# Performance work log

Measured on AMD Instinct MI355X. Metric: run time of the kernel, lower is better.

The kernel has to match this reference:

```python
import jax, jax.numpy as jnp
import numpy as np

D = 128      # internal_dimensions
L = 4        # num_edge_convs
N = 100000   # nodes
E = 800000   # edges
G = 64       # graphs
IN = 4       # in_channels


def _ln(x, g, b):
    m = jnp.mean(x, -1, keepdims=True)
    v = jnp.mean((x - m) ** 2, -1, keepdims=True)
    return (x - m) * jax.lax.rsqrt(v + 1e-5) * g + b


def _gelu(x):
    return jax.nn.gelu(x, approximate=False)  # torch nn.GELU default (erf)


def _seg_mean(x, seg, n):
    s = jax.ops.segment_sum(x, seg, num_segments=n)
    c = jax.ops.segment_sum(jnp.ones((x.shape[0], 1), x.dtype), seg, num_segments=n)
    return s / jnp.maximum(c, 1.0)


def _seg_max(x, seg, n):
    m = jax.ops.segment_max(x, seg, num_segments=n)
    return jnp.where(jnp.isfinite(m), m, 0.0)  # empty segments -> 0 (PyG convention)


def _forward(x, edge_index, batch, num_graphs,
             in_W1, in_b1, in_g1, in_bn1, in_W2, in_b2, in_g2, in_bn2,
             pre_g, pre_b, cW1, cb1, cg1, cbb1, cW2, cb2, cg2, cbb2, pW, pb,
             ag_g, ag_b,
             kW1, kb1, kg1, kbb1, kW2, kb2, kg2, kbb2,
             kW3, kb3, kg3, kbb3, kW4, kb4):
    n = x.shape[0]
    # input_net: Linear -> LN -> GELU -> Linear -> LN   (dropout=0, eval)
    h = _gelu(_ln(x @ in_W1 + in_b1, in_g1, in_bn1))
    h = _ln(h @ in_W2 + in_b2, in_g2, in_bn2)

    x_in_max = _seg_max(h, batch, num_graphs)
    x_in_mean = _seg_mean(h, batch, num_graphs)

    src, dst = edge_index[0], edge_index[1]  # PyG: message from src (x_j) to dst (x_i)
    xcur = h
    for l in range(L):
        identity = xcur
        hn = _ln(xcur, pre_g[l], pre_b[l])
        xi = hn[dst]            # [E, D]
        xj = hn[src]            # [E, D]
        m = jnp.concatenate([xi, xj - xi], axis=-1)       # [E, 2D]
        m = _gelu(_ln(m @ cW1[l] + cb1[l], cg1[l], cbb1[l]))
        m = _gelu(_ln(m @ cW2[l] + cb2[l], cg2[l], cbb2[l]))
        a_max = _seg_max(m, dst, n)
        a_mean = _seg_mean(m, dst, n)
        aggr = jnp.concatenate([a_max, a_mean], axis=-1)  # [N, 2D]
        xcur = identity + aggr @ pW[l] + pb[l]

    xcur = _ln(xcur, ag_g, ag_b)
    x_g_max = _seg_max(xcur, batch, num_graphs)
    x_g_mean = _seg_mean(xcur, batch, num_graphs)

    xp = jnp.concatenate([x_in_max, x_in_mean, x_g_max, x_g_mean], axis=-1)  # [G, 4D]
    z = _gelu(_ln(xp @ kW1 + kb1, kg1, kbb1))
    z = _gelu(_ln(z @ kW2 + kb2, kg2, kbb2))
    z = _gelu(_ln(z @ kW3 + kb3, kg3, kbb3))
    return z @ kW4 + kb4  # [G, 1]


def setup_inputs() -> dict:
    key = jax.random.key(0)
    ks = iter(jax.random.split(key, 64))
    def W(shape, fan):
        return jax.random.normal(next(ks), shape, jnp.float32) * np.float32((2.0 / fan) ** 0.5)
    inp = {}
    inp["x"] = jax.random.normal(next(ks), (N, IN), jnp.float32)
    inp["edge_index"] = jax.random.randint(next(ks), (2, E), 0, N)
    inp["batch"] = jnp.sort(jax.random.randint(next(ks), (N,), 0, G))
    inp["num_graphs"] = G
    inp["in_W1"] = W((IN, D), IN); inp["in_b1"] = jnp.zeros((D,), jnp.float32)
    inp["in_g1"] = jnp.ones((D,), jnp.float32); inp["in_bn1"] = jnp.zeros((D,), jnp.float32)
    inp["in_W2"] = W((D, D), D); inp["in_b2"] = jnp.zeros((D,), jnp.float32)
    inp["in_g2"] = jnp.ones((D,), jnp.float32); inp["in_bn2"] = jnp.zeros((D,), jnp.float32)
    inp["pre_g"] = jnp.ones((L, D), jnp.float32); inp["pre_b"] = jnp.zeros((L, D), jnp.float32)
    inp["cW1"] = W((L, 2 * D, D), 2 * D); inp["cb1"] = jnp.zeros((L, D), jnp.float32)
    inp["cg1"] = jnp.ones((L, D), jnp.float32); inp["cbb1"] = jnp.zeros((L, D), jnp.float32)
    inp["cW2"] = W((L, D, D), D); inp["cb2"] = jnp.zeros((L, D), jnp.float32)
    inp["cg2"] = jnp.ones((L, D), jnp.float32); inp["cbb2"] = jnp.zeros((L, D), jnp.float32)
    inp["pW"] = W((L, 2 * D, D), 2 * D); inp["pb"] = jnp.zeros((L, D), jnp.float32)
    inp["ag_g"] = jnp.ones((D,), jnp.float32); inp["ag_b"] = jnp.zeros((D,), jnp.float32)
    inp["kW1"] = W((4 * D, D), 4 * D); inp["kb1"] = jnp.zeros((D,), jnp.float32)
    inp["kg1"] = jnp.ones((D,), jnp.float32); inp["kbb1"] = jnp.zeros((D,), jnp.float32)
    inp["kW2"] = W((D, D), D); inp["kb2"] = jnp.zeros((D,), jnp.float32)
    inp["kg2"] = jnp.ones((D,), jnp.float32); inp["kbb2"] = jnp.zeros((D,), jnp.float32)
    inp["kW3"] = W((D, D // 4), D); inp["kb3"] = jnp.zeros((D // 4,), jnp.float32)
    inp["kg3"] = jnp.ones((D // 4,), jnp.float32); inp["kbb3"] = jnp.zeros((D // 4,), jnp.float32)
    inp["kW4"] = W((D // 4, 1), D // 4); inp["kb4"] = jnp.zeros((1,), jnp.float32)
    return inp


def reference(x, edge_index, batch, num_graphs,
              in_W1, in_b1, in_g1, in_bn1, in_W2, in_b2, in_g2, in_bn2,
              pre_g, pre_b, cW1, cb1, cg1, cbb1, cW2, cb2, cg2, cbb2, pW, pb,
              ag_g, ag_b,
              kW1, kb1, kg1, kbb1, kW2, kb2, kg2, kbb2,
              kW3, kb3, kg3, kbb3, kW4, kb4):
    return _forward(x, edge_index, batch, num_graphs,
                    in_W1, in_b1, in_g1, in_bn1, in_W2, in_b2, in_g2, in_bn2,
                    pre_g, pre_b, cW1, cb1, cg1, cbb1, cW2, cb2, cg2, cbb2, pW, pb,
                    ag_g, ag_b,
                    kW1, kb1, kg1, kbb1, kW2, kb2, kg2, kbb2,
                    kW3, kb3, kg3, kbb3, kW4, kb4)
```

## Files before the change

### kernel.cpp

```cpp
#include <hip/hip_runtime.h>
#include <hip/hip_bf16.h>
#include <math.h>

#define MAPNEGINF 0x007FFFFFu

__device__ __forceinline__ float geluf(float x) {
    return 0.5f * x * (1.0f + erff(x * 0.70710678118654752f));
}
__device__ __forceinline__ unsigned fmap(float f) {
    unsigned u = __float_as_uint(f);
    return ((int)u < 0) ? ~u : (u | 0x80000000u);
}
__device__ __forceinline__ float funmap(unsigned m) {
    return __uint_as_float((m & 0x80000000u) ? (m ^ 0x80000000u) : ~m);
}
__device__ __forceinline__ float wred64(float v) {
#pragma unroll
    for (int m = 1; m < 64; m <<= 1) v += __shfl_xor(v, m);
    return v;
}

__device__ __forceinline__ void stage_wq(float* Ws, const float* __restrict__ src, int t) {
#pragma unroll
    for (int it = 0; it < 4; ++it) {
        const int idx = it * 1024 + (t << 2);
        *(float4*)(Ws + idx) = *(const float4*)(src + idx);
    }
}

__device__ __forceinline__ void kloop_q(const float* As, const float* Ws, float (&acc)[4][8],
                                        const int r0, const int ogc, const int kb) {
#pragma unroll
    for (int kk = 0; kk < 32; kk += 4) {
        const float4 a0 = *(const float4*)(As + (r0 + 0) * 132 + kb + kk);
        const float4 a1 = *(const float4*)(As + (r0 + 1) * 132 + kb + kk);
        const float4 a2 = *(const float4*)(As + (r0 + 2) * 132 + kb + kk);
        const float4 a3 = *(const float4*)(As + (r0 + 3) * 132 + kb + kk);
#define MAD8(R, AV)                                                                     \
    {                                                                                   \
        acc[R][0] += (AV)*wA.x; acc[R][1] += (AV)*wA.y; acc[R][2] += (AV)*wA.z;         \
        acc[R][3] += (AV)*wA.w; acc[R][4] += (AV)*wB.x; acc[R][5] += (AV)*wB.y;         \
        acc[R][6] += (AV)*wB.z; acc[R][7] += (AV)*wB.w;                                 \
    }
#define KSTEP(J, C)                                                                     \
    {                                                                                   \
        const float4 wA = *(const float4*)(Ws + (kk + (J)) * 128 + ogc);                \
        const float4 wB = *(const float4*)(Ws + (kk + (J)) * 128 + 64 + ogc);           \
        MAD8(0, a0.C) MAD8(1, a1.C) MAD8(2, a2.C) MAD8(3, a3.C)                         \
    }
        KSTEP(0, x) KSTEP(1, y) KSTEP(2, z) KSTEP(3, w)
#undef KSTEP
#undef MAD8
    }
}

__global__ void k_zero(unsigned* __restrict__ p, int n) {
    const int i = blockIdx.x * 256 + threadIdx.x;
    if (i < n) p[i] = 0u;
}

__global__ void k_count(const int* __restrict__ ei, unsigned* __restrict__ deg, int E) {
    const int e = blockIdx.x * 256 + threadIdx.x;
    if (e < E) atomicAdd(deg + ei[E + e], 1u);
}

__global__ void k_scan1(const unsigned* __restrict__ deg, unsigned* __restrict__ excl,
                        unsigned* __restrict__ bsum, int n) {
    __shared__ unsigned sh[256];
    const int t = threadIdx.x;
    const int base = blockIdx.x * 1024 + t * 4;
    unsigned v0 = (base + 0 < n) ? deg[base + 0] : 0u;
    unsigned v1 = (base + 1 < n) ? deg[base + 1] : 0u;
    unsigned v2 = (base + 2 < n) ? deg[base + 2] : 0u;
    unsigned v3 = (base + 3 < n) ? deg[base + 3] : 0u;
    const unsigned s = v0 + v1 + v2 + v3;
    sh[t] = s;
    __syncthreads();
    for (int off = 1; off < 256; off <<= 1) {
        unsigned x = 0;
        if (t >= off) x = sh[t - off];
        __syncthreads();
        if (t >= off) sh[t] += x;
        __syncthreads();
    }
    const unsigned ebase = sh[t] - s;
    if (base + 0 < n) excl[base + 0] = ebase;
    if (base + 1 < n) excl[base + 1] = ebase + v0;
    if (base + 2 < n) excl[base + 2] = ebase + v0 + v1;
    if (base + 3 < n) excl[base + 3] = ebase + v0 + v1 + v2;
    if (t == 255) bsum[blockIdx.x] = sh[255];
}

__global__ void k_scan2(unsigned* __restrict__ bsum, int nb) {
    __shared__ unsigned sh[256];
    const int t = threadIdx.x;
    const unsigned v = (t < nb) ? bsum[t] : 0u;
    sh[t] = v;
    __syncthreads();
    for (int off = 1; off < 256; off <<= 1) {
        unsigned x = 0;
        if (t >= off) x = sh[t - off];
        __syncthreads();
        if (t >= off) sh[t] += x;
        __syncthreads();
    }
    if (t < nb) bsum[t] = sh[t] - v;
}

__global__ void k_scan3(unsigned* __restrict__ excl, const unsigned* __restrict__ bsum, int n) {
    const int t = threadIdx.x;
    const int base = blockIdx.x * 1024 + t * 4;
    const unsigned add = bsum[blockIdx.x];
#pragma unroll
    for (int j = 0; j < 4; ++j)
        if (base + j < n) excl[base + j] += add;
}

__global__ void k_scatter(const int* __restrict__ ei, unsigned* __restrict__ cursor,
                          int* __restrict__ eperm, int E) {
    const int e = blockIdx.x * 256 + threadIdx.x;
    if (e < E) {
        const unsigned pos = atomicAdd(cursor + ei[E + e], 1u);
        eperm[pos] = e;
    }
}

__global__ void k_in1(const float* __restrict__ x, const float* __restrict__ W1,
                      const float* __restrict__ b1, const float* __restrict__ g1,
                      const float* __restrict__ bn1, float* __restrict__ h, int n) {
    const int t = threadIdx.x, lane = t & 63, wave = t >> 6;
    const int d0 = lane << 1;
    const float2 w0 = *(const float2*)(W1 + d0);
    const float2 w1 = *(const float2*)(W1 + 128 + d0);
    const float2 w2 = *(const float2*)(W1 + 256 + d0);
    const float2 w3 = *(const float2*)(W1 + 384 + d0);
    const float2 bb = *(const float2*)(b1 + d0);
    const float2 gg = *(const float2*)(g1 + d0);
    const float2 nn = *(const float2*)(bn1 + d0);
    const int stride = gridDim.x * 4;
    for (int node = blockIdx.x * 4 + wave; node < n; node += stride) {
        const float4 xv = *(const float4*)(x + (size_t)node * 4);
        float h0 = bb.x + xv.x * w0.x + xv.y * w1.x + xv.z * w2.x + xv.w * w3.x;
        float h1 = bb.y + xv.x * w0.y + xv.y * w1.y + xv.z * w2.y + xv.w * w3.y;
        const float s = wred64(h0 + h1), q = wred64(h0 * h0 + h1 * h1);
        const float mean = s * 0.0078125f, var = q * 0.0078125f - mean * mean;
        const float rs = rsqrtf(var + 1e-5f);
        h0 = geluf((h0 - mean) * rs * gg.x + nn.x);
        h1 = geluf((h1 - mean) * rs * gg.y + nn.y);
        *(float2*)(h + (size_t)node * 128 + d0) = make_float2(h0, h1);
    }
}

__global__ __launch_bounds__(256, 2) void k_in2(const float* __restrict__ A,
                                                const float* __restrict__ W,
                                                const float* __restrict__ bias,
                                                const float* __restrict__ g,
                                                const float* __restrict__ b,
                                                float* __restrict__ C, int n) {
    __shared__ float As[64 * 132];
    __shared__ float Ws[4096];
    const int t = threadIdx.x;
    const int n0 = blockIdx.x * 64;
    {
        const int r = t >> 2, c0 = (t & 3) << 5;
        const int row = n0 + r;
        const bool ok = row < n;
#pragma unroll
        for (int j = 0; j < 8; ++j) {
            const int col = c0 + (j << 2);
            float4 v = make_float4(0.f, 0.f, 0.f, 0.f);
            if (ok) v = *(const float4*)(A + (size_t)row * 128 + col);
            *(float4*)(As + r * 132 + col) = v;
        }
    }
    float acc[4][8];
#pragma unroll
    for (int r = 0; r < 4; ++r)
#pragma unroll
        for (int o = 0; o < 8; ++o) acc[r][o] = 0.f;
    const int og = t & 15, eg = t >> 4;
    const int ogc = og << 2, r0 = eg << 2;
#pragma unroll
    for (int q4 = 0; q4 < 4; ++q4) {
        stage_wq(Ws, W + q4 * 4096, t);
        __syncthreads();
        kloop_q(As, Ws, acc, r0, ogc, q4 * 32);
        __syncthreads();
    }
    const float4 bA = *(const float4*)(bias + ogc);
    const float4 bB = *(const float4*)(bias + 64 + ogc);
    const float4 gA = *(const float4*)(g + ogc);
    const float4 gB = *(const float4*)(g + 64 + ogc);
    const float4 lA = *(const float4*)(b + ogc);
    const float4 lB = *(const float4*)(b + 64 + ogc);
#pragma unroll
    for (int r = 0; r < 4; ++r) {
        float v[8];
        v[0] = acc[r][0] + bA.x; v[1] = acc[r][1] + bA.y;
        v[2] = acc[r][2] + bA.z; v[3] = acc[r][3] + bA.w;
        v[4] = acc[r][4] + bB.x; v[5] = acc[r][5] + bB.y;
        v[6] = acc[r][6] + bB.z; v[7] = acc[r][7] + bB.w;
        float s = 0.f, q = 0.f;
#pragma unroll
        for (int o = 0; o < 8; ++o) { s += v[o]; q += v[o] * v[o]; }
#pragma unroll
        for (int m = 1; m < 16; m <<= 1) { s += __shfl_xor(s, m); q += __shfl_xor(q, m); }
        const float mean = s * 0.0078125f;
        const float var = q * 0.0078125f - mean * mean;
        const float rs = rsqrtf(var + 1e-5f);
        const int row = n0 + r0 + r;
        if (row < n) {
            *(float4*)(C + (size_t)row * 128 + ogc) = make_float4(
                (v[0] - mean) * rs * gA.x + lA.x, (v[1] - mean) * rs * gA.y + lA.y,
                (v[2] - mean) * rs * gA.z + lA.z, (v[3] - mean) * rs * gA.w + lA.w);
            *(float4*)(C + (size_t)row * 128 + 64 + ogc) = make_float4(
                (v[4] - mean) * rs * gB.x + lB.x, (v[5] - mean) * rs * gB.y + lB.y,
                (v[6] - mean) * rs * gB.z + lB.z, (v[7] - mean) * rs * gB.w + lB.w);
        }
    }
}

__global__ void k_ln(const float* __restrict__ in, const float* __restrict__ g,
                     const float* __restrict__ b, float* __restrict__ out, int n) {
    const int t = threadIdx.x, lane = t & 63, wave = t >> 6;
    const int d0 = lane << 1;
    const float ga = g[d0], gb = g[d0 + 1], ba = b[d0], bb = b[d0 + 1];
    const int stride = gridDim.x * 4;
    for (int node = blockIdx.x * 4 + wave; node < n; node += stride) {
        const float2 v = *(const float2*)(in + (size_t)node * 128 + d0);
        const float s = wred64(v.x + v.y), q = wred64(v.x * v.x + v.y * v.y);
        const float mean = s * 0.0078125f, var = q * 0.0078125f - mean * mean;
        const float rs = rsqrtf(var + 1e-5f);
        *(float2*)(out + (size_t)node * 128 + d0) =
            make_float2((v.x - mean) * rs * ga + ba, (v.y - mean) * rs * gb + bb);
    }
}

__global__ void k_wxj(const float* __restrict__ c, float* __restrict__ Wx,
                      float* __restrict__ Wj) {
    const int idx = blockIdx.x * 256 + threadIdx.x;
    const float a = c[idx], b = c[16384 + idx];
    Wx[idx] = a - b;
    Wj[idx] = b;
}

__global__ void k_fill(unsigned* __restrict__ amax, float* __restrict__ asum, int n4) {
    const uint4 mneg = make_uint4(MAPNEGINF, MAPNEGINF, MAPNEGINF, MAPNEGINF);
    const float4 z = make_float4(0.f, 0.f, 0.f, 0.f);
    for (int i = blockIdx.x * blockDim.x + threadIdx.x; i < n4; i += gridDim.x * blockDim.x) {
        ((uint4*)amax)[i] = mneg;
        ((float4*)asum)[i] = z;
    }
}

__global__ __launch_bounds__(256, 2) void k_pq(const float* __restrict__ xcur,
                                               const float* __restrict__ g,
                                               const float* __restrict__ b,
                                               const float* __restrict__ Wx,
                                               const float* __restrict__ Wj,
                                               const float* __restrict__ cb1,
                                               float* __restrict__ P, float* __restrict__ Q,
                                               int n) {
    __shared__ float As[64 * 132];
    __shared__ float Ws[4096];
    __shared__ float sg[128], sb[128];
    const int t = threadIdx.x;
    const int n0 = blockIdx.x * 64;
    if (t < 128) { sg[t] = g[t]; sb[t] = b[t]; }
    __syncthreads();
    {
        const int r = t >> 2, c0 = (t & 3) << 5;
        const int row = n0 + r;
        const bool ok = row < n;
        float4 v4[8];
        float s = 0.f, q = 0.f;
        if (ok) {
#pragma unroll
            for (int j = 0; j < 8; ++j) {
                v4[j] = *(const float4*)(xcur + (size_t)row * 128 + c0 + (j << 2));
                s += v4[j].x + v4[j].y + v4[j].z + v4[j].w;
                q += v4[j].x * v4[j].x + v4[j].y * v4[j].y + v4[j].z * v4[j].z +
                     v4[j].w * v4[j].w;
            }
        } else {
#pragma unroll
            for (int j = 0; j < 8; ++j) v4[j] = make_float4(0.f, 0.f, 0.f, 0.f);
        }
        s += __shfl_xor(s, 1); s += __shfl_xor(s, 2);
        q += __shfl_xor(q, 1); q += __shfl_xor(q, 2);
        const float mean = s * 0.0078125f;
        const float var = q * 0.0078125f - mean * mean;
        const float rs = rsqrtf(var + 1e-5f);
#pragma unroll
        for (int j = 0; j < 8; ++j) {
            const int c = c0 + (j << 2);
            As[r * 132 + c + 0] = (v4[j].x - mean) * rs * sg[c + 0] + sb[c + 0];
            As[r * 132 + c + 1] = (v4[j].y - mean) * rs * sg[c + 1] + sb[c + 1];
            As[r * 132 + c + 2] = (v4[j].z - mean) * rs * sg[c + 2] + sb[c + 2];
            As[r * 132 + c + 3] = (v4[j].w - mean) * rs * sg[c + 3] + sb[c + 3];
        }
    }
    float accP[4][8], accQ[4][8];
#pragma unroll
    for (int r = 0; r < 4; ++r)
#pragma unroll
        for (int o = 0; o < 8; ++o) { accP[r][o] = 0.f; accQ[r][o] = 0.f; }
    const int og = t & 15, eg = t >> 4;
    const int ogc = og << 2, r0 = eg << 2;
#pragma unroll
    for (int q4 = 0; q4 < 4; ++q4) {
        stage_wq(Ws, Wx + q4 * 4096, t);
        __syncthreads();
        kloop_q(As, Ws, accP, r0, ogc, q4 * 32);
        __syncthreads();
    }
#pragma unroll
    for (int q4 = 0; q4 < 4; ++q4) {
        stage_wq(Ws, Wj + q4 * 4096, t);
        __syncthreads();
        kloop_q(As, Ws, accQ, r0, ogc, q4 * 32);
        __syncthreads();
    }
    const float4 bA = *(const float4*)(cb1 + ogc);
    const float4 bB = *(const float4*)(cb1 + 64 + ogc);
#pragma unroll
    for (int r = 0; r < 4; ++r) {
        const int row = n0 + r0 + r;
        if (row < n) {
            *(float4*)(P + (size_t)row * 128 + ogc) =
                make_float4(accP[r][0] + bA.x, accP[r][1] + bA.y, accP[r][2] + bA.z,
                            accP[r][3] + bA.w);
            *(float4*)(P + (size_t)row * 128 + 64 + ogc) =
                make_float4(accP[r][4] + bB.x, accP[r][5] + bB.y, accP[r][6] + bB.z,
                            accP[r][7] + bB.w);
            *(float4*)(Q + (size_t)row * 128 + ogc) =
                make_float4(accQ[r][0], accQ[r][1], accQ[r][2], accQ[r][3]);
            *(float4*)(Q + (size_t)row * 128 + 64 + ogc) =
                make_float4(accQ[r][4], accQ[r][5], accQ[r][6], accQ[r][7]);
        }
    }
}

__global__ __launch_bounds__(256, 2) void k_edge(
    const float* __restrict__ P, const float* __restrict__ Q, const int* __restrict__ ei,
    const int* __restrict__ eperm, const float* __restrict__ W2, const float* __restrict__ g1,
    const float* __restrict__ b1, const float* __restrict__ cb2, const float* __restrict__ g2,
    const float* __restrict__ b2, unsigned* __restrict__ amax, float* __restrict__ asum, int E) {
    __shared__ float Us[64 * 132];
    __shared__ float Ws[4096];
    __shared__ int sdst[64], ssrc[64], sdg[64];
    __shared__ float scb2[128], sg2[128], sb2[128];
    const int t = threadIdx.x;
    const int base = blockIdx.x * 64;
    if (base >= E) return;
    if (t < 64) {
        const int idx = base + t;
        const int e = eperm[idx < E ? idx : (E - 1)];
        ssrc[t] = ei[e];
        const int d = ei[E + e];
        sdg[t] = d;
        sdst[t] = (idx < E) ? d : -1;
    }
    if (t >= 128) {
        const int d = t - 128;
        scb2[d] = cb2[d];
        sg2[d] = g2[d];
        sb2[d] = b2[d];
    }
    __syncthreads();
    const int lane = t & 63, wave = t >> 6;
    const int d0 = lane << 1;
    const float g1a = g1[d0], g1b = g1[d0 + 1], b1a = b1[d0], b1b = b1[d0 + 1];
#pragma unroll 2
    for (int p = 0; p < 16; ++p) {
        const int i = (p << 2) + wave;
        const int nd = sdg[i], ns = ssrc[i];
        const float2 pv = *(const float2*)(P + (size_t)nd * 128 + d0);
        const float2 qv = *(const float2*)(Q + (size_t)ns * 128 + d0);
        const float x0 = pv.x + qv.x, x1 = pv.y + qv.y;
        const float s = wred64(x0 + x1);
        const float q = wred64(x0 * x0 + x1 * x1);
        const float mean = s * 0.0078125f;
        const float var = q * 0.0078125f - mean * mean;
        const float rs = rsqrtf(var + 1e-5f);
        const float y0 = geluf((x0 - mean) * rs * g1a + b1a);
        const float y1 = geluf((x1 - mean) * rs * g1b + b1b);
        *(float2*)(Us + i * 132 + d0) = make_float2(y0, y1);
    }
    float acc[4][8];
#pragma unroll
    for (int r = 0; r < 4; ++r)
#pragma unroll
        for (int o = 0; o < 8; ++o) acc[r][o] = 0.f;
    const int og = t & 15, eg = t >> 4;
    const int ogc = og << 2, r0 = eg << 2;
#pragma unroll
    for (int q4 = 0; q4 < 4; ++q4) {
        stage_wq(Ws, W2 + q4 * 4096, t);
        __syncthreads();
        kloop_q(Us, Ws, acc, r0, ogc, q4 * 32);
        __syncthreads();
    }
#pragma unroll
    for (int r = 0; r < 4; ++r) {
        float v[8];
        float s = 0.f, q = 0.f;
#pragma unroll
        for (int o = 0; o < 8; ++o) {
            const int col = (o < 4) ? (ogc + o) : (64 + ogc + o - 4);
            v[o] = acc[r][o] + scb2[col];
            s += v[o];
            q += v[o] * v[o];
        }
#pragma unroll
        for (int m = 1; m < 16; m <<= 1) { s += __shfl_xor(s, m); q += __shfl_xor(q, m); }
        const float mean = s * 0.0078125f;
        const float var = q * 0.0078125f - mean * mean;
        const float rs = rsqrtf(var + 1e-5f);
#pragma unroll
        for (int o = 0; o < 8; ++o) {
            const int col = (o < 4) ? (ogc + o) : (64 + ogc + o - 4);
            v[o] = geluf((v[o] - mean) * rs * sg2[col] + sb2[col]);
        }
        *(float4*)(Us + (r0 + r) * 132 + ogc) = make_float4(v[0], v[1], v[2], v[3]);
        *(float4*)(Us + (r0 + r) * 132 + 64 + ogc) = make_float4(v[4], v[5], v[6], v[7]);
    }
    __syncthreads();
    if (t < 128) {
        int cur = sdst[0];
        float vmax = -INFINITY, vsum = 0.f;
        for (int i = 0; i < 64; ++i) {
            const int dn = sdst[i];
            if (dn != cur) {
                if (cur >= 0) {
                    atomicMax(amax + (size_t)cur * 128 + t, fmap(vmax));
                    atomicAdd(asum + (size_t)cur * 128 + t, vsum);
                }
                cur = dn;
                vmax = -INFINITY;
                vsum = 0.f;
            }
            const float v = Us[i * 132 + t];
            vmax = fmaxf(vmax, v);
            vsum += v;
        }
        if (cur >= 0) {
            atomicMax(amax + (size_t)cur * 128 + t, fmap(vmax));
            atomicAdd(asum + (size_t)cur * 128 + t, vsum);
        }
    }
}

__global__ __launch_bounds__(256, 2) void k_update(const unsigned* __restrict__ amax,
                                                   const float* __restrict__ asum,
                                                   const unsigned* __restrict__ deg,
                                                   const float* __restrict__ pW,
                                                   const float* __restrict__ pb,
                                                   float* __restrict__ xcur, int n) {
    __shared__ float As[64 * 132];
    __shared__ float Ws[4096];
    const int t = threadIdx.x;
    const int n0 = blockIdx.x * 64;
    const int og = t & 15, eg = t >> 4;
    const int ogc = og << 2, r0 = eg << 2;
    float acc[4][8];
#pragma unroll
    for (int r = 0; r < 4; ++r)
#pragma unroll
        for (int o = 0; o < 8; ++o) acc[r][o] = 0.f;
    const int r = t >> 2, c0 = (t & 3) << 5;
    const int row = n0 + r;
    const bool ok = row < n;
#pragma unroll
    for (int pass = 0; pass < 2; ++pass) {
        if (pass == 0) {
#pragma unroll
            for (int j = 0; j < 8; ++j) {
                const int col = c0 + (j << 2);
                float4 v = make_float4(0.f, 0.f, 0.f, 0.f);
                if (ok) {
                    const uint4 u = *(const uint4*)(amax + (size_t)row * 128 + col);
                    v.x = (u.x == MAPNEGINF) ? 0.f : funmap(u.x);
                    v.y = (u.y == MAPNEGINF) ? 0.f : funmap(u.y);
                    v.z = (u.z == MAPNEGINF) ? 0.f : funmap(u.z);
                    v.w = (u.w == MAPNEGINF) ? 0.f : funmap(u.w);
                }
                *(float4*)(As + r * 132 + col) = v;
            }
        } else {
            float inv = 0.f;
            if (ok) {
                const unsigned dv = deg[row];
                inv = 1.f / (float)(dv < 1u ? 1u : dv);
            }
#pragma unroll
            for (int j = 0; j < 8; ++j) {
                const int col = c0 + (j << 2);
                float4 v = make_float4(0.f, 0.f, 0.f, 0.f);
                if (ok) {
                    const float4 sv = *(const float4*)(asum + (size_t)row * 128 + col);
                    v = make_float4(sv.x * inv, sv.y * inv, sv.z * inv, sv.w * inv);
                }
                *(float4*)(As + r * 132 + col) = v;
            }
        }
#pragma unroll
        for (int q4 = 0; q4 < 4; ++q4) {
            stage_wq(Ws, pW + (size_t)(pass * 128 + q4 * 32) * 128, t);
            __syncthreads();
            kloop_q(As, Ws, acc, r0, ogc, q4 * 32);
            __syncthreads();
        }
    }
    const float4 bA = *(const float4*)(pb + ogc);
    const float4 bB = *(const float4*)(pb + 64 + ogc);
#pragma unroll
    for (int rr = 0; rr < 4; ++rr) {
        const int orow = n0 + r0 + rr;
        if (orow < n) {
            const float4 x0 = *(const float4*)(xcur + (size_t)orow * 128 + ogc);
            const float4 x1 = *(const float4*)(xcur + (size_t)orow * 128 + 64 + ogc);
            *(float4*)(xcur + (size_t)orow * 128 + ogc) =
                make_float4(x0.x + acc[rr][0] + bA.x, x0.y + acc[rr][1] + bA.y,
                            x0.z + acc[rr][2] + bA.z, x0.w + acc[rr][3] + bA.w);
            *(float4*)(xcur + (size_t)orow * 128 + 64 + ogc) =
                make_float4(x1.x + acc[rr][4] + bB.x, x1.y + acc[rr][5] + bB.y,
                            x1.z + acc[rr][6] + bB.z, x1.w + acc[rr][7] + bB.w);
        }
    }
}

__global__ void k_pool_init(unsigned* __restrict__ gmax1, float* __restrict__ gsum1,
                            unsigned* __restrict__ gcount1, unsigned* __restrict__ gmax2,
                            float* __restrict__ gsum2, unsigned* __restrict__ gcount2, int ng) {
    const int i = blockIdx.x * 256 + threadIdx.x;
    if (i < ng * 128) {
        gmax1[i] = MAPNEGINF;
        gsum1[i] = 0.f;
        gmax2[i] = MAPNEGINF;
        gsum2[i] = 0.f;
    }
    if (i < ng) {
        gcount1[i] = 0u;
        gcount2[i] = 0u;
    }
}

__global__ void k_pool(const float* __restrict__ in, const int* __restrict__ batch,
                       unsigned* __restrict__ gmax, float* __restrict__ gsum,
                       unsigned* __restrict__ gcount, int n) {
    const int t = threadIdx.x;
    if (t >= 128) return;
    const int per = (n + gridDim.x - 1) / gridDim.x;
    const int i0 = blockIdx.x * per;
    const int i1 = min(n, i0 + per);
    if (i0 >= i1) return;
    int cur = batch[i0];
    float vmax = -INFINITY, vsum = 0.f;
    unsigned cnt = 0;
    for (int i = i0; i < i1; ++i) {
        const int g = batch[i];
        if (g != cur) {
            atomicMax(gmax + (size_t)cur * 128 + t, fmap(vmax));
            atomicAdd(gsum + (size_t)cur * 128 + t, vsum);
            if (t == 0) atomicAdd(gcount + cur, cnt);
            cur = g;
            vmax = -INFINITY;
            vsum = 0.f;
            cnt = 0;
        }
        const float v = in[(size_t)i * 128 + t];
        vmax = fmaxf(vmax, v);
        vsum += v;
        cnt++;
    }
    atomicMax(gmax + (size_t)cur * 128 + t, fmap(vmax));
    atomicAdd(gsum + (size_t)cur * 128 + t, vsum);
    if (t == 0) atomicAdd(gcount + cur, cnt);
}

__global__ void k_xp(const unsigned* __restrict__ gmax1, const float* __restrict__ gsum1,
                     const unsigned* __restrict__ gcount1, const unsigned* __restrict__ gmax2,
                     const float* __restrict__ gsum2, const unsigned* __restrict__ gcount2,
                     float* __restrict__ xp) {
    const int g = blockIdx.x, d = threadIdx.x;
    const unsigned c1u = gcount1[g], c2u = gcount2[g];
    const float c1 = (float)(c1u < 1u ? 1u : c1u);
    const float c2 = (float)(c2u < 1u ? 1u : c2u);
    const unsigned m1 = gmax1[g * 128 + d], m2 = gmax2[g * 128 + d];
    xp[g * 512 + d] = (m1 == MAPNEGINF) ? 0.f : funmap(m1);
    xp[g * 512 + 128 + d] = gsum1[g * 128 + d] / c1;
    xp[g * 512 + 256 + d] = (m2 == MAPNEGINF) ? 0.f : funmap(m2);
    xp[g * 512 + 384 + d] = gsum2[g * 128 + d] / c2;
}

__global__ __launch_bounds__(64) void k_know(
    const float* __restrict__ xp, const float* __restrict__ kW1, const float* __restrict__ kb1,
    const float* __restrict__ kg1, const float* __restrict__ kbb1, const float* __restrict__ kW2,
    const float* __restrict__ kb2, const float* __restrict__ kg2, const float* __restrict__ kbb2,
    const float* __restrict__ kW3, const float* __restrict__ kb3, const float* __restrict__ kg3,
    const float* __restrict__ kbb3, const float* __restrict__ kW4, const float* __restrict__ kb4,
    float* __restrict__ out) {
    __shared__ float sh[512];
    __shared__ float s3[32];
    const int l = threadIdx.x, g = blockIdx.x;
    const int d0 = l << 1;
    *(float4*)(sh + l * 8) = *(const float4*)(xp + g * 512 + l * 8);
    *(float4*)(sh + l * 8 + 4) = *(const float4*)(xp + g * 512 + l * 8 + 4);
    __syncthreads();
    float a0 = kb1[d0], a1 = kb1[d0 + 1];
    for (int k = 0; k < 512; ++k) {
        const float u = sh[k];
        const float2 w = *(const float2*)(kW1 + k * 128 + d0);
        a0 += u * w.x;
        a1 += u * w.y;
    }
    {
        const float s = wred64(a0 + a1), q = wred64(a0 * a0 + a1 * a1);
        const float mean = s * 0.0078125f, var = q * 0.0078125f - mean * mean;
        const float rs = rsqrtf(var + 1e-5f);
        a0 = geluf((a0 - mean) * rs * kg1[d0] + kbb1[d0]);
        a1 = geluf((a1 - mean) * rs * kg1[d0 + 1] + kbb1[d0 + 1]);
    }
    __syncthreads();
    sh[d0] = a0;
    sh[d0 + 1] = a1;
    __syncthreads();
    float b0v = kb2[d0], b1v = kb2[d0 + 1];
    for (int k = 0; k < 128; ++k) {
        const float u = sh[k];
        const float2 w = *(const float2*)(kW2 + k * 128 + d0);
        b0v += u * w.x;
        b1v += u * w.y;
    }
    {
        const float s = wred64(b0v + b1v), q = wred64(b0v * b0v + b1v * b1v);
        const float mean = s * 0.0078125f, var = q * 0.0078125f - mean * mean;
        const float rs = rsqrtf(var + 1e-5f);
        b0v = geluf((b0v - mean) * rs * kg2[d0] + kbb2[d0]);
        b1v = geluf((b1v - mean) * rs * kg2[d0 + 1] + kbb2[d0 + 1]);
    }
    __syncthreads();
    sh[d0] = b0v;
    sh[d0 + 1] = b1v;
    __syncthreads();
    const int d3 = (l & 15) << 1;
    float c0 = kb3[d3], c1 = kb3[d3 + 1];
    for (int k = 0; k < 128; ++k) {
        const float u = sh[k];
        const float2 w = *(const float2*)(kW3 + k * 32 + d3);
        c0 += u * w.x;
        c1 += u * w.y;
    }
    {
        float s = c0 + c1, q = c0 * c0 + c1 * c1;
#pragma unroll
        for (int m = 1; m < 16; m <<= 1) {
            s += __shfl_xor(s, m);
            q += __shfl_xor(q, m);
        }
        const float mean = s * 0.03125f, var = q * 0.03125f - mean * mean;
        const float rs = rsqrtf(var + 1e-5f);
        c0 = geluf((c0 - mean) * rs * kg3[d3] + kbb3[d3]);
        c1 = geluf((c1 - mean) * rs * kg3[d3 + 1] + kbb3[d3 + 1]);
    }
    if (l < 16) {
        s3[d3] = c0;
        s3[d3 + 1] = c1;
    }
    __syncthreads();
    if (l == 0) {
        float rr = kb4[0];
        for (int k = 0; k < 32; ++k) rr += s3[k] * kW4[k];
        out[g] = rr;
    }
}

extern "C" void kernel_launch(void* const* d_in, const int* in_sizes, int n_in, void* d_out,
                              int out_size, void* d_ws, size_t ws_size, hipStream_t stream) {
    const int N = in_sizes[0] / 4;
    const int E = in_sizes[1] / 2;
    const int G = 64;
    const int L = 4;

    const float* x = (const float*)d_in[0];
    const int* ei = (const int*)d_in[1];
    const int* batch = (const int*)d_in[2];
    const float* inW1 = (const float*)d_in[4];
    const float* inb1 = (const float*)d_in[5];
    const float* ing1 = (const float*)d_in[6];
    const float* inbn1 = (const float*)d_in[7];
    const float* inW2 = (const float*)d_in[8];
    const float* inb2 = (const float*)d_in[9];
    const float* ing2 = (const float*)d_in[10];
    const float* inbn2 = (const float*)d_in[11];
    const float* pre_g = (const float*)d_in[12];
    const float* pre_b = (const float*)d_in[13];
    const float* cW1 = (const float*)d_in[14];
    const float* cb1 = (const float*)d_in[15];
    const float* cg1 = (const float*)d_in[16];
    const float* cbb1 = (const float*)d_in[17];
    const float* cW2 = (const float*)d_in[18];
    const float* cb2 = (const float*)d_in[19];
    const float* cg2 = (const float*)d_in[20];
    const float* cbb2 = (const float*)d_in[21];
    const float* pW = (const float*)d_in[22];
    const float* pb = (const float*)d_in[23];
    const float* ag_g = (const float*)d_in[24];
    const float* ag_b = (const float*)d_in[25];
    const float* kW1 = (const float*)d_in[26];
    const float* kb1 = (const float*)d_in[27];
    const float* kg1 = (const float*)d_in[28];
    const float* kbb1 = (const float*)d_in[29];
    const float* kW2 = (const float*)d_in[30];
    const float* kb2 = (const float*)d_in[31];
    const float* kg2 = (const float*)d_in[32];
    const float* kbb2 = (const float*)d_in[33];
    const float* kW3 = (const float*)d_in[34];
    const float* kb3 = (const float*)d_in[35];
    const float* kg3 = (const float*)d_in[36];
    const float* kbb3 = (const float*)d_in[37];
    const float* kW4 = (const float*)d_in[38];
    const float* kb4 = (const float*)d_in[39];
    float* out = (float*)d_out;

    char* wsb = (char*)d_ws;
    size_t off = 0;
    auto ALC = [&](size_t bytes) {
        void* p = wsb + off;
        off = (off + bytes + 255) & ~(size_t)255;
        return p;
    };
    const size_t NB = (size_t)N * 128 * 4;
    float* xcur = (float*)ALC(NB);
    float* Pb = (float*)ALC(NB);
    float* Qb = (float*)ALC(NB);
    unsigned* amax = (unsigned*)ALC(NB);
    float* asum = (float*)ALC(NB);
    unsigned* deg = (unsigned*)ALC((size_t)N * 4);
    unsigned* cursor = (unsigned*)ALC((size_t)N * 4);
    unsigned* bsum = (unsigned*)ALC(4096);
    int* eperm = (int*)ALC((size_t)E * 4);
    float* Wx = (float*)ALC(65536);
    float* Wj = (float*)ALC(65536);
    unsigned* gmax1 = (unsigned*)ALC((size_t)G * 128 * 4);
    float* gsum1 = (float*)ALC((size_t)G * 128 * 4);
    unsigned* gcount1 = (unsigned*)ALC((size_t)G * 4);
    unsigned* gmax2 = (unsigned*)ALC((size_t)G * 128 * 4);
    float* gsum2 = (float*)ALC((size_t)G * 128 * 4);
    unsigned* gcount2 = (unsigned*)ALC((size_t)G * 4);
    float* xp = (float*)ALC((size_t)G * 512 * 4);

    if (off > ws_size) {
        k_zero<<<(out_size + 255) / 256, 256, 0, stream>>>((unsigned*)d_out, out_size);
        return;
    }

    k_zero<<<(N + 255) / 256, 256, 0, stream>>>(deg, N);
    k_count<<<(E + 255) / 256, 256, 0, stream>>>(ei, deg, E);
    const int nb = (N + 1023) / 1024;
    k_scan1<<<nb, 256, 0, stream>>>(deg, cursor, bsum, N);
    k_scan2<<<1, 256, 0, stream>>>(bsum, nb);
    k_scan3<<<nb, 256, 0, stream>>>(cursor, bsum, N);
    k_scatter<<<(E + 255) / 256, 256, 0, stream>>>(ei, cursor, eperm, E);

    const int gemmGrid = (N + 63) / 64;
    k_in1<<<1024, 256, 0, stream>>>(x, inW1, inb1, ing1, inbn1, Pb, N);
    k_in2<<<gemmGrid, 256, 0, stream>>>(Pb, inW2, inb2, ing2, inbn2, xcur, N);
    k_pool_init<<<(G * 128 + 255) / 256, 256, 0, stream>>>(gmax1, gsum1, gcount1, gmax2, gsum2,
                                                           gcount2, G);
    k_pool<<<512, 256, 0, stream>>>(xcur, batch, gmax1, gsum1, gcount1, N);

    for (int l = 0; l < L; ++l) {
        k_wxj<<<64, 256, 0, stream>>>(cW1 + (size_t)l * 32768, Wx, Wj);
        k_pq<<<gemmGrid, 256, 0, stream>>>(xcur, pre_g + l * 128, pre_b + l * 128, Wx, Wj,
                                           cb1 + l * 128, Pb, Qb, N);
        k_fill<<<2048, 256, 0, stream>>>(amax, asum, N * 32);
        k_edge<<<(E + 63) / 64, 256, 0, stream>>>(Pb, Qb, ei, eperm, cW2 + (size_t)l * 16384,
                                                  cg1 + l * 128, cbb1 + l * 128, cb2 + l * 128,
                                                  cg2 + l * 128, cbb2 + l * 128, amax, asum, E);
        k_update<<<gemmGrid, 256, 0, stream>>>(amax, asum, deg, pW + (size_t)l * 32768,
                                               pb + l * 128, xcur, N);
    }

    k_ln<<<1024, 256, 0, stream>>>(xcur, ag_g, ag_b, Pb, N);
    k_pool<<<512, 256, 0, stream>>>(Pb, batch, gmax2, gsum2, gcount2, N);
    k_xp<<<G, 128, 0, stream>>>(gmax1, gsum1, gcount1, gmax2, gsum2, gcount2, xp);
    k_know<<<G, 64, 0, stream>>>(xp, kW1, kb1, kg1, kbb1, kW2, kb2, kg2, kbb2, kW3, kb3, kg3, kbb3,
                                 kW4, kb4, out);
}
```

Before: 91.76 ms.

## Replace atomic segment aggregation with per-block partial records and merge kernel

Each edge block now processes 512 CSR-sorted edges in eight 64-edge sub-tiles. A node whose edge range lies entirely inside one block gets its max and sum written directly, and boundary nodes write partial records that a new merge kernel combines. This removes the fill kernel, the atomicMax/atomicAdd traffic and the float-to-ordered-uint mapping. It also batches the P/Q gathers eight at a time per wave to expose memory parallelism, and raises launch bounds to 3 blocks per CU. The risks are register spilling under the tighter bound, longer serial per-block loops, and an extra merge pass over all nodes.

Result: slower. 102.0 ms (+11.1%).

```diff
diff --git a/kernel.cpp b/kernel.cpp
--- a/kernel.cpp
+++ b/kernel.cpp
@@ -2,8 +2,6 @@
 #include <hip/hip_bf16.h>
 #include <math.h>
 
-#define MAPNEGINF 0x007FFFFFu
-
 __device__ __forceinline__ float geluf(float x) {
     return 0.5f * x * (1.0f + erff(x * 0.70710678118654752f));
 }
@@ -14,6 +12,7 @@
 __device__ __forceinline__ float funmap(unsigned m) {
     return __uint_as_float((m & 0x80000000u) ? (m ^ 0x80000000u) : ~m);
 }
+#define MAPNEGINF 0x007FFFFFu
 __device__ __forceinline__ float wred64(float v) {
 #pragma unroll
     for (int m = 1; m < 64; m <<= 1) v += __shfl_xor(v, m);
@@ -57,6 +56,15 @@
 __global__ void k_zero(unsigned* __restrict__ p, int n) {
     const int i = blockIdx.x * 256 + threadIdx.x;
     if (i < n) p[i] = 0u;
+}
+
+__global__ void k_copyu(const unsigned* __restrict__ a, const unsigned* __restrict__ b,
+                        unsigned* __restrict__ ac, unsigned* __restrict__ bc, int n) {
+    const int i = blockIdx.x * 256 + threadIdx.x;
+    if (i < n) {
+        ac[i] = a[i];
+        bc[i] = b[i];
+    }
 }
 
 __global__ void k_count(const int* __restrict__ ei, unsigned* __restrict__ deg, int E) {
@@ -151,7 +159,7 @@
     }
 }
 
-__global__ __launch_bounds__(256, 2) void k_in2(const float* __restrict__ A,
+__global__ __launch_bounds__(256, 3) void k_in2(const float* __restrict__ A,
                                                 const float* __restrict__ W,
                                                 const float* __restrict__ bias,
                                                 const float* __restrict__ g,
@@ -244,16 +252,7 @@
     Wj[idx] = b;
 }
 
-__global__ void k_fill(unsigned* __restrict__ amax, float* __restrict__ asum, int n4) {
-    const uint4 mneg = make_uint4(MAPNEGINF, MAPNEGINF, MAPNEGINF, MAPNEGINF);
-    const float4 z = make_float4(0.f, 0.f, 0.f, 0.f);
-    for (int i = blockIdx.x * blockDim.x + threadIdx.x; i < n4; i += gridDim.x * blockDim.x) {
-        ((uint4*)amax)[i] = mneg;
-        ((float4*)asum)[i] = z;
-    }
-}
-
-__global__ __launch_bounds__(256, 2) void k_pq(const float* __restrict__ xcur,
+__global__ __launch_bounds__(256, 3) void k_pq(const float* __restrict__ xcur,
                                                const float* __restrict__ g,
                                                const float* __restrict__ b,
                                                const float* __restrict__ Wx,
@@ -341,119 +340,197 @@
     }
 }
 
-__global__ __launch_bounds__(256, 2) void k_edge(
+__global__ __launch_bounds__(256, 3) void k_edge(
     const float* __restrict__ P, const float* __restrict__ Q, const int* __restrict__ ei,
     const int* __restrict__ eperm, const float* __restrict__ W2, const float* __restrict__ g1,
     const float* __restrict__ b1, const float* __restrict__ cb2, const float* __restrict__ g2,
-    const float* __restrict__ b2, unsigned* __restrict__ amax, float* __restrict__ asum, int E) {
+    const float* __restrict__ b2, const unsigned* __restrict__ rowend,
+    const unsigned* __restrict__ degc, float* __restrict__ amax, float* __restrict__ asum,
+    float* __restrict__ recmax, float* __restrict__ recsum, int* __restrict__ recid, int E) {
     __shared__ float Us[64 * 132];
     __shared__ float Ws[4096];
     __shared__ int sdst[64], ssrc[64], sdg[64];
     __shared__ float scb2[128], sg2[128], sb2[128];
     const int t = threadIdx.x;
-    const int base = blockIdx.x * 64;
-    if (base >= E) return;
-    if (t < 64) {
-        const int idx = base + t;
-        const int e = eperm[idx < E ? idx : (E - 1)];
-        ssrc[t] = ei[e];
-        const int d = ei[E + e];
-        sdg[t] = d;
-        sdst[t] = (idx < E) ? d : -1;
-    }
+    const int base = blockIdx.x * 512;
     if (t >= 128) {
         const int d = t - 128;
         scb2[d] = cb2[d];
         sg2[d] = g2[d];
         sb2[d] = b2[d];
     }
-    __syncthreads();
     const int lane = t & 63, wave = t >> 6;
     const int d0 = lane << 1;
     const float g1a = g1[d0], g1b = g1[d0 + 1], b1a = b1[d0], b1b = b1[d0 + 1];
-#pragma unroll 2
-    for (int p = 0; p < 16; ++p) {
-        const int i = (p << 2) + wave;
-        const int nd = sdg[i], ns = ssrc[i];
-        const float2 pv = *(const float2*)(P + (size_t)nd * 128 + d0);
-        const float2 qv = *(const float2*)(Q + (size_t)ns * 128 + d0);
-        const float x0 = pv.x + qv.x, x1 = pv.y + qv.y;
-        const float s = wred64(x0 + x1);
-        const float q = wred64(x0 * x0 + x1 * x1);
-        const float mean = s * 0.0078125f;
-        const float var = q * 0.0078125f - mean * mean;
-        const float rs = rsqrtf(var + 1e-5f);
-        const float y0 = geluf((x0 - mean) * rs * g1a + b1a);
-        const float y1 = geluf((x1 - mean) * rs * g1b + b1b);
-        *(float2*)(Us + i * 132 + d0) = make_float2(y0, y1);
-    }
-    float acc[4][8];
-#pragma unroll
-    for (int r = 0; r < 4; ++r)
-#pragma unroll
-        for (int o = 0; o < 8; ++o) acc[r][o] = 0.f;
     const int og = t & 15, eg = t >> 4;
     const int ogc = og << 2, r0 = eg << 2;
-#pragma unroll
-    for (int q4 = 0; q4 < 4; ++q4) {
-        stage_wq(Ws, W2 + q4 * 4096, t);
-        __syncthreads();
-        kloop_q(Us, Ws, acc, r0, ogc, q4 * 32);
-        __syncthreads();
-    }
-#pragma unroll
-    for (int r = 0; r < 4; ++r) {
-        float v[8];
-        float s = 0.f, q = 0.f;
-#pragma unroll
-        for (int o = 0; o < 8; ++o) {
-            const int col = (o < 4) ? (ogc + o) : (64 + ogc + o - 4);
-            v[o] = acc[r][o] + scb2[col];
-            s += v[o];
-            q += v[o] * v[o];
-        }
-#pragma unroll
-        for (int m = 1; m < 16; m <<= 1) { s += __shfl_xor(s, m); q += __shfl_xor(q, m); }
-        const float mean = s * 0.0078125f;
-        const float var = q * 0.0078125f - mean * mean;
-        const float rs = rsqrtf(var + 1e-5f);
-#pragma unroll
-        for (int o = 0; o < 8; ++o) {
-            const int col = (o < 4) ? (ogc + o) : (64 + ogc + o - 4);
-            v[o] = geluf((v[o] - mean) * rs * sg2[col] + sb2[col]);
-        }
-        *(float4*)(Us + (r0 + r) * 132 + ogc) = make_float4(v[0], v[1], v[2], v[3]);
-        *(float4*)(Us + (r0 + r) * 132 + 64 + ogc) = make_float4(v[4], v[5], v[6], v[7]);
-    }
-    __syncthreads();
-    if (t < 128) {
-        int cur = sdst[0];
-        float vmax = -INFINITY, vsum = 0.f;
-        for (int i = 0; i < 64; ++i) {
-            const int dn = sdst[i];
-            if (dn != cur) {
-                if (cur >= 0) {
-                    atomicMax(amax + (size_t)cur * 128 + t, fmap(vmax));
-                    atomicAdd(asum + (size_t)cur * 128 + t, vsum);
+    int cur = -1, istart = 0;
+    float vmax = -INFINITY, vsum = 0.f;
+    int id0 = -1, id1 = -1;
+
+    for (int s8 = 0; s8 < 8; ++s8) {
+        const int sb = base + s8 * 64;
+        __syncthreads();
+        if (t < 64) {
+            const int idx = sb + t;
+            const int e = eperm[idx < E ? idx : (E - 1)];
+            ssrc[t] = ei[e];
+            const int d = ei[E + e];
+            sdg[t] = d;
+            sdst[t] = (idx < E) ? d : -1;
+        }
+        __syncthreads();
+#pragma unroll
+        for (int half = 0; half < 2; ++half) {
+            float2 pv[8], qv[8];
+#pragma unroll
+            for (int u = 0; u < 8; ++u) {
+                const int i = ((half * 8 + u) << 2) + wave;
+                pv[u] = *(const float2*)(P + (size_t)sdg[i] * 128 + d0);
+                qv[u] = *(const float2*)(Q + (size_t)ssrc[i] * 128 + d0);
+            }
+#pragma unroll
+            for (int u = 0; u < 8; ++u) {
+                const int i = ((half * 8 + u) << 2) + wave;
+                const float x0 = pv[u].x + qv[u].x, x1 = pv[u].y + qv[u].y;
+                const float s = wred64(x0 + x1);
+                const float q = wred64(x0 * x0 + x1 * x1);
+                const float mean = s * 0.0078125f;
+                const float var = q * 0.0078125f - mean * mean;
+                const float rs = rsqrtf(var + 1e-5f);
+                const float y0 = geluf((x0 - mean) * rs * g1a + b1a);
+                const float y1 = geluf((x1 - mean) * rs * g1b + b1b);
+                *(float2*)(Us + i * 132 + d0) = make_float2(y0, y1);
+            }
+        }
+        float acc[4][8];
+#pragma unroll
+        for (int r = 0; r < 4; ++r)
+#pragma unroll
+            for (int o = 0; o < 8; ++o) acc[r][o] = 0.f;
+#pragma unroll
+        for (int q4 = 0; q4 < 4; ++q4) {
+            stage_wq(Ws, W2 + q4 * 4096, t);
+            __syncthreads();
+            kloop_q(Us, Ws, acc, r0, ogc, q4 * 32);
+            __syncthreads();
+        }
+#pragma unroll
+        for (int r = 0; r < 4; ++r) {
+            float v[8];
+            float s = 0.f, q = 0.f;
+#pragma unroll
+            for (int o = 0; o < 8; ++o) {
+                const int col = (o < 4) ? (ogc + o) : (64 + ogc + o - 4);
+                v[o] = acc[r][o] + scb2[col];
+                s += v[o];
+                q += v[o] * v[o];
+            }
+#pragma unroll
+            for (int m = 1; m < 16; m <<= 1) { s += __shfl_xor(s, m); q += __shfl_xor(q, m); }
+            const float mean = s * 0.0078125f;
+            const float var = q * 0.0078125f - mean * mean;
+            const float rs = rsqrtf(var + 1e-5f);
+#pragma unroll
+            for (int o = 0; o < 8; ++o) {
+                const int col = (o < 4) ? (ogc + o) : (64 + ogc + o - 4);
+                v[o] = geluf((v[o] - mean) * rs * sg2[col] + sb2[col]);
+            }
+            *(float4*)(Us + (r0 + r) * 132 + ogc) = make_float4(v[0], v[1], v[2], v[3]);
+            *(float4*)(Us + (r0 + r) * 132 + 64 + ogc) = make_float4(v[4], v[5], v[6], v[7]);
+        }
+        __syncthreads();
+        if (t < 128) {
+            for (int i = 0; i < 64; ++i) {
+                const int dn = sdst[i];
+                const int gi = s8 * 64 + i;
+                if (dn != cur) {
+                    if (cur >= 0) {
+                        const unsigned re = rowend[cur];
+                        const unsigned rs0 = re - degc[cur];
+                        const unsigned ps = (unsigned)(base + istart);
+                        const unsigned pe = (unsigned)(base + gi);
+                        if (ps == rs0 && pe == re) {
+                            amax[(size_t)cur * 128 + t] = vmax;
+                            asum[(size_t)cur * 128 + t] = vsum;
+                        } else {
+                            const int slot = (istart == 0) ? 0 : 1;
+                            const size_t ro = (size_t)(2 * blockIdx.x + slot) * 128 + t;
+                            recmax[ro] = vmax;
+                            recsum[ro] = vsum;
+                            if (slot == 0) id0 = cur; else id1 = cur;
+                        }
+                    }
+                    cur = dn;
+                    istart = gi;
+                    vmax = -INFINITY;
+                    vsum = 0.f;
                 }
-                cur = dn;
-                vmax = -INFINITY;
-                vsum = 0.f;
-            }
-            const float v = Us[i * 132 + t];
-            vmax = fmaxf(vmax, v);
-            vsum += v;
-        }
-        if (cur >= 0) {
-            atomicMax(amax + (size_t)cur * 128 + t, fmap(vmax));
-            atomicAdd(asum + (size_t)cur * 128 + t, vsum);
-        }
-    }
-}
-
-__global__ __launch_bounds__(256, 2) void k_update(const unsigned* __restrict__ amax,
+                if (dn >= 0) {
+                    const float v = Us[i * 132 + t];
+                    vmax = fmaxf(vmax, v);
+                    vsum += v;
+                }
+            }
+        }
+    }
+    if (t < 128 && cur >= 0) {
+        const int iend = min(512, E - base);
+        const unsigned re = rowend[cur];
+        const unsigned rs0 = re - degc[cur];
+        const unsigned ps = (unsigned)(base + istart);
+        const unsigned pe = (unsigned)(base + iend);
+        if (ps == rs0 && pe == re) {
+            amax[(size_t)cur * 128 + t] = vmax;
+            asum[(size_t)cur * 128 + t] = vsum;
+        } else {
+            const int slot = (istart == 0) ? 0 : 1;
+            const size_t ro = (size_t)(2 * blockIdx.x + slot) * 128 + t;
+            recmax[ro] = vmax;
+            recsum[ro] = vsum;
+            if (slot == 0) id0 = cur; else id1 = cur;
+        }
+    }
+    if (t == 0) {
+        recid[2 * blockIdx.x] = id0;
+        recid[2 * blockIdx.x + 1] = id1;
+    }
+}
+
+__global__ void k_merge(const unsigned* __restrict__ rowend, const unsigned* __restrict__ degc,
+                        const float* __restrict__ recmax, const float* __restrict__ recsum,
+                        const int* __restrict__ recid, float* __restrict__ amax,
+                        float* __restrict__ asum, int n) {
+    const int node = blockIdx.x * 2 + (threadIdx.x >> 7);
+    const int t = threadIdx.x & 127;
+    if (node >= n) return;
+    const unsigned dg = degc[node];
+    if (dg == 0u) {
+        amax[(size_t)node * 128 + t] = 0.f;
+        asum[(size_t)node * 128 + t] = 0.f;
+        return;
+    }
+    const unsigned re = rowend[node], rs = re - dg;
+    const int b0 = rs >> 9, b1 = (re - 1) >> 9;
+    if (b0 == b1) return;
+    float m = -INFINITY, s = 0.f;
+    for (int b = b0; b <= b1; ++b) {
+#pragma unroll
+        for (int sl = 0; sl < 2; ++sl) {
+            if (recid[2 * b + sl] == node) {
+                const size_t ro = (size_t)(2 * b + sl) * 128 + t;
+                m = fmaxf(m, recmax[ro]);
+                s += recsum[ro];
+            }
+        }
+    }
+    amax[(size_t)node * 128 + t] = m;
+    asum[(size_t)node * 128 + t] = s;
+}
+
+__global__ __launch_bounds__(256, 3) void k_update(const float* __restrict__ amax,
                                                    const float* __restrict__ asum,
-                                                   const unsigned* __restrict__ deg,
+                                                   const unsigned* __restrict__ degc,
                                                    const float* __restrict__ pW,
                                                    const float* __restrict__ pb,
                                                    float* __restrict__ xcur, int n) {
@@ -478,19 +555,13 @@
             for (int j = 0; j < 8; ++j) {
                 const int col = c0 + (j << 2);
                 float4 v = make_float4(0.f, 0.f, 0.f, 0.f);
-                if (ok) {
-                    const uint4 u = *(const uint4*)(amax + (size_t)row * 128 + col);
-                    v.x = (u.x == MAPNEGINF) ? 0.f : funmap(u.x);
-                    v.y = (u.y == MAPNEGINF) ? 0.f : funmap(u.y);
-                    v.z = (u.z == MAPNEGINF) ? 0.f : funmap(u.z);
-                    v.w = (u.w == MAPNEGINF) ? 0.f : funmap(u.w);
-                }
+                if (ok) v = *(const float4*)(amax + (size_t)row * 128 + col);
                 *(float4*)(As + r * 132 + col) = v;
             }
         } else {
             float inv = 0.f;
             if (ok) {
-                const unsigned dv = deg[row];
+                const unsigned dv = degc[row];
                 inv = 1.f / (float)(dv < 1u ? 1u : dv);
             }
 #pragma unroll
@@ -724,6 +795,8 @@
     const float* kb4 = (const float*)d_in[39];
     float* out = (float*)d_out;
 
+    const int nblkE = (E + 511) / 512;
+
     char* wsb = (char*)d_ws;
     size_t off = 0;
     auto ALC = [&](size_t bytes) {
@@ -735,12 +808,17 @@
     float* xcur = (float*)ALC(NB);
     float* Pb = (float*)ALC(NB);
     float* Qb = (float*)ALC(NB);
-    unsigned* amax = (unsigned*)ALC(NB);
+    float* amax = (float*)ALC(NB);
     float* asum = (float*)ALC(NB);
     unsigned* deg = (unsigned*)ALC((size_t)N * 4);
     unsigned* cursor = (unsigned*)ALC((size_t)N * 4);
+    unsigned* degc = (unsigned*)ALC((size_t)N * 4);
+    unsigned* rowend = (unsigned*)ALC((size_t)N * 4);
     unsigned* bsum = (unsigned*)ALC(4096);
     int* eperm = (int*)ALC((size_t)E * 4);
+    float* recmax = (float*)ALC((size_t)nblkE * 2 * 128 * 4);
+    float* recsum = (float*)ALC((size_t)nblkE * 2 * 128 * 4);
+    int* recid = (int*)ALC((size_t)nblkE * 2 * 4);
     float* Wx = (float*)ALC(65536);
     float* Wj = (float*)ALC(65536);
     unsigned* gmax1 = (unsigned*)ALC((size_t)G * 128 * 4);
@@ -763,6 +841,7 @@
     k_scan2<<<1, 256, 0, stream>>>(bsum, nb);
     k_scan3<<<nb, 256, 0, stream>>>(cursor, bsum, N);
     k_scatter<<<(E + 255) / 256, 256, 0, stream>>>(ei, cursor, eperm, E);
+    k_copyu<<<(N + 255) / 256, 256, 0, stream>>>(deg, cursor, degc, rowend, N);
 
     const int gemmGrid = (N + 63) / 64;
     k_in1<<<1024, 256, 0, stream>>>(x, inW1, inb1, ing1, inbn1, Pb, N);
@@ -775,17 +854,19 @@
         k_wxj<<<64, 256, 0, stream>>>(cW1 + (size_t)l * 32768, Wx, Wj);
         k_pq<<<gemmGrid, 256, 0, stream>>>(xcur, pre_g + l * 128, pre_b + l * 128, Wx, Wj,
                                            cb1 + l * 128, Pb, Qb, N);
-        k_fill<<<2048, 256, 0, stream>>>(amax, asum, N * 32);
-        k_edge<<<(E + 63) / 64, 256, 0, stream>>>(Pb, Qb, ei, eperm, cW2 + (size_t)l * 16384,
-                                                  cg1 + l * 128, cbb1 + l * 128, cb2 + l * 128,
-                                                  cg2 + l * 128, cbb2 + l * 128, amax, asum, E);
-        k_update<<<gemmGrid, 256, 0, stream>>>(amax, asum, deg, pW + (size_t)l * 32768,
+        k_edge<<<nblkE, 256, 0, stream>>>(Pb, Qb, ei, eperm, cW2 + (size_t)l * 16384,
+                                          cg1 + l * 128, cbb1 + l * 128, cb2 + l * 128,
+                                          cg2 + l * 128, cbb2 + l * 128, rowend, degc, amax, asum,
+                                          recmax, recsum, recid, E);
+        k_merge<<<(N + 1) / 2, 256, 0, stream>>>(rowend, degc, recmax, recsum, recid, amax, asum,
+                                                 N);
+        k_update<<<gemmGrid, 256, 0, stream>>>(amax, asum, degc, pW + (size_t)l * 32768,
                                                pb + l * 128, xcur, N);
     }
 
     k_ln<<<1024, 256, 0, stream>>>(xcur, ag_g, ag_b, Pb, N);
     k_pool<<<512, 256, 0, stream>>>(Pb, batch, gmax2, gsum2, gcount2, N);
     k_xp<<<G, 128, 0, stream>>>(gmax1, gsum1, gcount1, gmax2, gsum2, gcount2, xp);
-    k_know<<<G, 64, 0, stream>>>(xp, kW1, kb1, kg1, kbb1, kW2, kb2, kg2, kbb2, kW3, kb3, kg3, kbb3,
-                                 kW4, kb4, out);
-}
+    k_know<<<G, 64, 0, stream>>>(xp, kW1, kb1, kg1, kbb1, kW2, kb2, kg2, kbb2, kW3, kb3, kg3,
+                                 kbb3, kW4, kb4, out);
+}
```
